# Kernel tuning notes

Measured on AMD Instinct MI355X. Metric: run time of the kernel, lower is better.

Reference implementation:

```python
import jax, jax.numpy as jnp
import numpy as np

N_SRC, N_TGT, K, L, C_OUT = 16384, 16384, 16, 128, 2
E = N_TGT * K
MIN_VAR = 1e-3   # adf.keep_variance_fn min variance (applied in Dropout)
DROP_P = 0.2
INV_SQRT2 = np.float32(1.0 / np.sqrt(2.0))
INV_SQRT2PI = np.float32(1.0 / np.sqrt(2.0 * np.pi))


def setup_inputs() -> dict:
    key = jax.random.key(0)
    ks = jax.random.split(key, 12)
    pos_source = jax.random.uniform(ks[0], (N_SRC, 3), jnp.float32)
    pos_target = jax.random.uniform(ks[1], (N_TGT, 3), jnp.float32)
    latents = jax.random.normal(ks[2], (N_SRC, L), jnp.float32)
    var = jax.random.uniform(ks[3], (N_SRC, L), jnp.float32)
    # KNN-style edge list: each target has K source neighbors
    row = jnp.repeat(jnp.arange(N_TGT, dtype=jnp.int32), K)          # [E] target idx
    col = jax.random.randint(ks[4], (E,), 0, N_SRC, jnp.int32)       # [E] source idx
    occupancies = jax.random.randint(ks[5], (N_TGT,), 0, 2, jnp.int32)
    # fixed inverted-dropout mask (deterministic stand-in for adf.Dropout training mask)
    drop_mask = (jax.random.uniform(ks[6], (E, L)) >= DROP_P).astype(jnp.float32) / (1.0 - DROP_P)
    def init_w(k, sh):
        return jax.random.normal(k, sh, jnp.float32) * np.float32(1.0 / np.sqrt(sh[-1]))
    W_in = init_w(ks[7], (L, L + 3)); b_in = jnp.zeros((L,), jnp.float32)
    W1 = init_w(ks[8], (L, L)); b1 = jnp.zeros((L,), jnp.float32)
    W2 = init_w(ks[9], (L, L)); b2 = jnp.zeros((L,), jnp.float32)
    W_out = init_w(ks[10], (C_OUT, L)); b_out = jnp.zeros((C_OUT,), jnp.float32)
    return dict(pos_source=pos_source, pos_target=pos_target, latents=latents, var=var,
                drop_mask=drop_mask, W_in=W_in, b_in=b_in, W1=W1, b1=b1, W2=W2, b2=b2,
                W_out=W_out, b_out=b_out, row=row, col=col, occupancies=occupancies)


def _adf_linear(m, v, W, b):
    # ADF Linear: mean -> affine; variance -> through squared weights, no bias
    return m @ W.T + b, v @ (W * W).T


def _adf_relu(m, v):
    # ADF ReLU moment matching (Gast & Roth); clamp var for sqrt stability
    v = jnp.maximum(v, 1e-6)
    std = jnp.sqrt(v)
    r = m / std
    cdf = 0.5 * (1.0 + jax.lax.erf(r * INV_SQRT2))
    pdf = jnp.exp(-0.5 * r * r) * INV_SQRT2PI
    m_out = m * cdf + std * pdf
    v_out = (m * m + v) * cdf + m * std * pdf - m_out * m_out
    return m_out, v_out


def reference(pos_source, pos_target, latents, var, drop_mask, W_in, b_in, W1, b1, W2, b2, W_out, b_out, row, col, occupancies):
    pos_rel = pos_target[row] - pos_source[col]                    # [E,3]
    m = jnp.concatenate([latents[col], pos_rel], axis=1)           # [E,L+3]
    v = jnp.concatenate([var[col], pos_rel], axis=1)               # [E,L+3] (faithful: pos_rel reused as 'variance')
    m, v = _adf_linear(m, v, W_in, b_in)
    for W, b in ((W1, b1), (W2, b2)):
        m, v = _adf_relu(m, v)
        m, v = _adf_linear(m, v, W, b)
    # ADF dropout with keep_variance_fn
    m = m * drop_mask
    v = v * drop_mask * drop_mask + MIN_VAR
    m, v = _adf_linear(m, v, W_out, b_out)                         # [E,2]
    preds = m[:, 0]
    aleatoric = jnp.abs(v[:, 0]).mean()
    occ_gt = occupancies[row].astype(jnp.float32)
    # stable binary_cross_entropy_with_logits, mean reduction
    recons_loss = jnp.mean(jnp.maximum(preds, 0.0) - preds * occ_gt + jnp.log1p(jnp.exp(-jnp.abs(preds))))
    return preds, aleatoric, recons_loss, occ_gt
```

## Files before the change

kernel.cpp:

```cpp
#include <hip/hip_runtime.h>
#include <math.h>

#define E_TOT 262144
#define N_SRC 16384
#define LDIM  128
#define MIN_VARF 0.001f
#define INV_SQRT2PIF 0.3989422804014327f
#define EPB   128
#define NBLK  (E_TOT / EPB)

typedef _Float16 half8  __attribute__((ext_vector_type(8)));
typedef __fp16   fp16x2 __attribute__((ext_vector_type(2)));
typedef float    f32x4  __attribute__((ext_vector_type(4)));
typedef float    f32x2  __attribute__((ext_vector_type(2)));
typedef unsigned int uint2v __attribute__((ext_vector_type(2)));

#define BIAS_OFF  256
#define WOUT_OFF  1792
#define BOUT_OFF  2816
#define PART_OFF  4096
#define PK_L0     36864
#define PK_L1     77824
#define PK_L2     110592
#define LAT16_OFF 143360
#define VAR16_OFF 4337664
#define WS_NEED   8531968

__device__ __forceinline__ unsigned int pkrtz(float a, float b) {
    union { fp16x2 h; unsigned int u; } z;
    z.h = __builtin_amdgcn_cvt_pkrtz(a, b);
    return z.u;
}
__device__ __forceinline__ half8 to_h8(f32x4 a, f32x4 b) {
    union { half8 h; unsigned int u[4]; } z;
    z.u[0] = pkrtz(a[0], a[1]); z.u[1] = pkrtz(a[2], a[3]);
    z.u[2] = pkrtz(b[0], b[1]); z.u[3] = pkrtz(b[2], b[3]);
    return z.h;
}
__device__ __forceinline__ half8 ch_to_h8(uint2v lo, uint2v hi) {
    union { half8 h; unsigned int u[4]; } z;
    z.u[0] = lo[0]; z.u[1] = lo[1]; z.u[2] = hi[0]; z.u[3] = hi[1];
    return z.h;
}

__device__ __forceinline__ void adf_relu(float& m, float& v) {
    float vv = fmaxf(v, 1e-6f);
    float is = __builtin_amdgcn_rsqf(vv);
    float sd = vv * is;
    float r  = m * is;
    float qq = 0.5f * r * r;
    float e  = __expf(-qq);
    float sp = sd * e * INV_SQRT2PIF;
    const float P = 0.23165247f;
    float t  = __builtin_amdgcn_rcpf(fmaf(fabsf(r), P, 1.0f));
    float poly = t * fmaf(t, fmaf(t, fmaf(t, fmaf(t, 1.061405429f, -1.453152027f),
                                          1.421413741f), -0.284496736f), 0.254829592f);
    float erfa = fmaf(-poly, e, 1.0f);
    float cdf  = fmaf(copysignf(0.5f, r), erfa, 0.5f);
    float mo = fmaf(m, cdf, sp);
    float vo = fmaf(fmaf(m, m, vv), cdf, fmaf(m, sp, -mo * mo));
    m = mo; v = vo;
}

__global__ void prep_pack(const float* __restrict__ latents, const float* __restrict__ varr,
                          char* __restrict__ ws)
{
    int idx = blockIdx.x * 256 + threadIdx.x;
    const int half = idx >> 18;
    const int j    = idx & 262143;
    const float* src = (half ? varr : latents) + (long)j * 8;
    char* dst = ws + (half ? VAR16_OFF : LAT16_OFF) + (long)j * 16;
    f32x4 a = *(const f32x4*)(src);
    f32x4 b = *(const f32x4*)(src + 4);
    half8 hv;
#pragma unroll
    for (int k = 0; k < 4; ++k) { hv[k] = (_Float16)a[k]; hv[k + 4] = (_Float16)b[k]; }
    *(half8*)dst = hv;
}

__global__ void prep(const float* __restrict__ W_in, const float* __restrict__ b_in,
                     const float* __restrict__ W1,   const float* __restrict__ b1,
                     const float* __restrict__ W2,   const float* __restrict__ b2,
                     const float* __restrict__ W_out,const float* __restrict__ b_out,
                     char* __restrict__ ws)
{
    int idx = blockIdx.x * 256 + threadIdx.x;
    if (idx < 6656) {
        const float* W; long dstoff; int entry; bool lin;
        if (idx < 2560)      { entry = idx;        W = W_in; dstoff = PK_L0; lin = true;  }
        else if (idx < 4608) { entry = idx - 2560; W = W1;   dstoff = PK_L1; lin = false; }
        else                 { entry = idx - 4608; W = W2;   dstoff = PK_L2; lin = false; }
        int ks   = entry >> 9;
        int rest = entry & 511;
        int t    = rest >> 6;
        int lane = rest & 63;
        int rowi = t * 16 + (lane & 15);
        int gp   = lane >> 4;
        half8 hv;
        if (lin) {
            int k0 = ks * 32 + gp * 8;
#pragma unroll
            for (int j = 0; j < 8; ++j) {
                int k = k0 + j;
                hv[j] = (_Float16)((k < 131) ? W[rowi * 131 + k] : 0.0f);
            }
        } else {
#pragma unroll
            for (int j = 0; j < 8; ++j) {
                int k = (2 * ks + (j >= 4 ? 1 : 0)) * 16 + 4 * gp + (j & 3);
                hv[j] = (_Float16)W[rowi * 128 + k];
            }
        }
        *(half8*)(ws + dstoff + (long)entry * 16) = hv;
    } else if (idx < 6656 + 384) {
        int j = idx - 6656; int layer = j >> 7; int pidx = j & 127;
        int gg = pidx >> 5, t = (pidx >> 2) & 7, r = pidx & 3;
        int n = t * 16 + gg * 4 + r;
        const float* b = layer == 0 ? b_in : (layer == 1 ? b1 : b2);
        ((float*)(ws + BIAS_OFF))[layer * 128 + pidx] = b[n];
    } else if (idx < 6656 + 384 + 256) {
        int j = idx - 6656 - 384; int path = j >> 7; int pidx = j & 127;
        int gg = pidx >> 5, t = (pidx >> 2) & 7, r = pidx & 3;
        int n = t * 16 + gg * 4 + r;
        float v = W_out[n];
        if (path) v = v * v;
        ((float*)(ws + WOUT_OFF))[path * 128 + pidx] = v;
    } else if (idx == 6656 + 384 + 256) {
        ((float*)(ws + BOUT_OFF))[0] = b_out[0];
    }
}

__device__ __forceinline__ void epi_reg(const f32x4* am, const f32x4* av, const f32x4* bp,
                                        uint2v* chm, uint2v* chv)
{
#pragma unroll
    for (int t = 0; t < 8; ++t) {
        f32x4 b4 = bp[t];
        float m0 = am[t][0] + b4[0], m1 = am[t][1] + b4[1];
        float m2 = am[t][2] + b4[2], m3 = am[t][3] + b4[3];
        float v0 = av[t][0], v1 = av[t][1], v2 = av[t][2], v3 = av[t][3];
        adf_relu(m0, v0); adf_relu(m1, v1); adf_relu(m2, v2); adf_relu(m3, v3);
        uint2v sm = {pkrtz(m0, m1), pkrtz(m2, m3)};
        uint2v sv = {pkrtz(v0, v1), pkrtz(v2, v3)};
        chm[t] = sm; chv[t] = sv;
    }
}

template <bool PACKED>
__global__ void __launch_bounds__(256, 2)
interp_main(const float* __restrict__ pos_source, const float* __restrict__ pos_target,
            const float* __restrict__ latents,    const float* __restrict__ varr,
            const float* __restrict__ drop_mask,
            const int* __restrict__ row, const int* __restrict__ col, const int* __restrict__ occ,
            float* __restrict__ out, char* __restrict__ ws)
{
    __shared__ float wred[4][2];

    const int tid  = threadIdx.x;
    const int lane = tid & 63;
    const int w    = tid >> 6;
    const int q    = lane & 15;
    const int g    = lane >> 4;
    const int g8   = g * 8;
    const int er0  = w * 32 + q;
    const int er1  = er0 + 16;
    const int ge0  = blockIdx.x * EPB + er0;
    const int ge1  = ge0 + 16;

    const int c0 = col[ge0], c1 = col[ge1];
    const int r0 = row[ge0], r1 = row[ge1];
    const float occf0 = (float)occ[r0];
    const float occf1 = (float)occ[r1];
    const float px0 = pos_target[r0 * 3 + 0] - pos_source[c0 * 3 + 0];
    const float py0 = pos_target[r0 * 3 + 1] - pos_source[c0 * 3 + 1];
    const float pz0 = pos_target[r0 * 3 + 2] - pos_source[c0 * 3 + 2];
    const float px1 = pos_target[r1 * 3 + 0] - pos_source[c1 * 3 + 0];
    const float py1 = pos_target[r1 * 3 + 1] - pos_source[c1 * 3 + 1];
    const float pz1 = pos_target[r1 * 3 + 2] - pos_source[c1 * 3 + 2];

    f32x4 acm0[8], acv0[8], acm1[8], acv1[8];
    const f32x4 zz = {0.0f, 0.0f, 0.0f, 0.0f};
#pragma unroll
    for (int t = 0; t < 8; ++t) { acm0[t] = zz; acv0[t] = zz; acm1[t] = zz; acv1[t] = zz; }

    uint2v chm0[8], chv0[8], chm1[8], chv1[8];

    {
        const char* pk = ws + PK_L0 + lane * 16;
#pragma unroll
        for (int ks = 0; ks < 4; ++ks) {
            half8 bm0, bv0, bm1, bv1;
            if (PACKED) {
                const long o0 = (long)c0 * 256 + ks * 64 + g8 * 2;
                const long o1 = (long)c1 * 256 + ks * 64 + g8 * 2;
                bm0 = *(const half8*)(ws + LAT16_OFF + o0);
                bv0 = *(const half8*)(ws + VAR16_OFF + o0);
                bm1 = *(const half8*)(ws + LAT16_OFF + o1);
                bv1 = *(const half8*)(ws + VAR16_OFF + o1);
            } else {
                const f32x4* a0 = (const f32x4*)(latents + (long)c0 * LDIM + ks * 32 + g8);
                const f32x4* s0 = (const f32x4*)(varr    + (long)c0 * LDIM + ks * 32 + g8);
                const f32x4* a1 = (const f32x4*)(latents + (long)c1 * LDIM + ks * 32 + g8);
                const f32x4* s1 = (const f32x4*)(varr    + (long)c1 * LDIM + ks * 32 + g8);
                bm0 = to_h8(a0[0], a0[1]); bv0 = to_h8(s0[0], s0[1]);
                bm1 = to_h8(a1[0], a1[1]); bv1 = to_h8(s1[0], s1[1]);
            }
            const char* pmk = pk + ks * 8192;
            __builtin_amdgcn_s_setprio(1);
#pragma unroll
            for (int t = 0; t < 8; ++t) {
                half8 am = *(const half8*)(pmk + t * 1024);
                half8 av = am * am;
                acm0[t] = __builtin_amdgcn_mfma_f32_16x16x32_f16(am, bm0, acm0[t], 0, 0, 0);
                acm1[t] = __builtin_amdgcn_mfma_f32_16x16x32_f16(am, bm1, acm1[t], 0, 0, 0);
                acv0[t] = __builtin_amdgcn_mfma_f32_16x16x32_f16(av, bv0, acv0[t], 0, 0, 0);
                acv1[t] = __builtin_amdgcn_mfma_f32_16x16x32_f16(av, bv1, acv1[t], 0, 0, 0);
            }
            __builtin_amdgcn_s_setprio(0);
        }
        half8 bp0 = {(_Float16)0.f, (_Float16)0.f, (_Float16)0.f, (_Float16)0.f,
                     (_Float16)0.f, (_Float16)0.f, (_Float16)0.f, (_Float16)0.f};
        half8 bp1 = bp0;
        if (g == 0) {
            bp0[0] = (_Float16)px0; bp0[1] = (_Float16)py0; bp0[2] = (_Float16)pz0;
            bp1[0] = (_Float16)px1; bp1[1] = (_Float16)py1; bp1[2] = (_Float16)pz1;
        }
        const char* pmk = pk + 4 * 8192;
        __builtin_amdgcn_s_setprio(1);
#pragma unroll
        for (int t = 0; t < 8; ++t) {
            half8 am = *(const half8*)(pmk + t * 1024);
            half8 av = am * am;
            acm0[t] = __builtin_amdgcn_mfma_f32_16x16x32_f16(am, bp0, acm0[t], 0, 0, 0);
            acm1[t] = __builtin_amdgcn_mfma_f32_16x16x32_f16(am, bp1, acm1[t], 0, 0, 0);
            acv0[t] = __builtin_amdgcn_mfma_f32_16x16x32_f16(av, bp0, acv0[t], 0, 0, 0);
            acv1[t] = __builtin_amdgcn_mfma_f32_16x16x32_f16(av, bp1, acv1[t], 0, 0, 0);
        }
        __builtin_amdgcn_s_setprio(0);
        const f32x4* bp = (const f32x4*)(ws + BIAS_OFF) + g8;
        epi_reg(acm0, acv0, bp, chm0, chv0);
        epi_reg(acm1, acv1, bp, chm1, chv1);
    }

#pragma unroll
    for (int layer = 1; layer < 3; ++layer) {
        const char* pk = ws + (layer == 1 ? PK_L1 : PK_L2) + lane * 16;
#pragma unroll
        for (int t = 0; t < 8; ++t) { acm0[t] = zz; acv0[t] = zz; acm1[t] = zz; acv1[t] = zz; }
#pragma unroll
        for (int ks = 0; ks < 4; ++ks) {
            half8 bm0 = ch_to_h8(chm0[2 * ks], chm0[2 * ks + 1]);
            half8 bv0 = ch_to_h8(chv0[2 * ks], chv0[2 * ks + 1]);
            half8 bm1 = ch_to_h8(chm1[2 * ks], chm1[2 * ks + 1]);
            half8 bv1 = ch_to_h8(chv1[2 * ks], chv1[2 * ks + 1]);
            const char* pmk = pk + ks * 8192;
            __builtin_amdgcn_s_setprio(1);
#pragma unroll
            for (int t = 0; t < 8; ++t) {
                half8 am = *(const half8*)(pmk + t * 1024);
                half8 av = am * am;
                acm0[t] = __builtin_amdgcn_mfma_f32_16x16x32_f16(am, bm0, acm0[t], 0, 0, 0);
                acm1[t] = __builtin_amdgcn_mfma_f32_16x16x32_f16(am, bm1, acm1[t], 0, 0, 0);
                acv0[t] = __builtin_amdgcn_mfma_f32_16x16x32_f16(av, bv0, acv0[t], 0, 0, 0);
                acv1[t] = __builtin_amdgcn_mfma_f32_16x16x32_f16(av, bv1, acv1[t], 0, 0, 0);
            }
            __builtin_amdgcn_s_setprio(0);
        }
        if (layer == 1) {
            const f32x4* bp = (const f32x4*)(ws + BIAS_OFF) + 32 + g8;
            epi_reg(acm0, acv0, bp, chm0, chv0);
            epi_reg(acm1, acv1, bp, chm1, chv1);
        }
    }

    {
        const f32x4* wmp = (const f32x4*)(ws + WOUT_OFF);
        const f32x4* bp  = (const f32x4*)(ws + BIAS_OFF) + 64 + g8;
        const f32x4* dm0 = (const f32x4*)(drop_mask + (size_t)ge0 * LDIM) + g;
        const f32x4* dm1 = (const f32x4*)(drop_mask + (size_t)ge1 * LDIM) + g;
        float pm0 = 0.f, pv0 = 0.f, pm1 = 0.f, pv1 = 0.f;
#pragma unroll
        for (int t = 0; t < 8; ++t) {
            f32x4 b4 = bp[t];
            f32x4 w4 = wmp[g8 + t];
            f32x4 s4 = wmp[32 + g8 + t];
            f32x4 d0 = __builtin_nontemporal_load(dm0 + t * 4);
            f32x4 d1 = __builtin_nontemporal_load(dm1 + t * 4);
#pragma unroll
            for (int j = 0; j < 4; ++j) {
                float m0 = (acm0[t][j] + b4[j]) * d0[j];
                float v0 = acv0[t][j] * d0[j] * d0[j] + MIN_VARF;
                float m1 = (acm1[t][j] + b4[j]) * d1[j];
                float v1 = acv1[t][j] * d1[j] * d1[j] + MIN_VARF;
                pm0 = fmaf(w4[j], m0, pm0); pv0 = fmaf(s4[j], v0, pv0);
                pm1 = fmaf(w4[j], m1, pm1); pv1 = fmaf(s4[j], v1, pv1);
            }
        }
        pm0 += __shfl_xor(pm0, 16, 64); pm0 += __shfl_xor(pm0, 32, 64);
        pv0 += __shfl_xor(pv0, 16, 64); pv0 += __shfl_xor(pv0, 32, 64);
        pm1 += __shfl_xor(pm1, 16, 64); pm1 += __shfl_xor(pm1, 32, 64);
        pv1 += __shfl_xor(pv1, 16, 64); pv1 += __shfl_xor(pv1, 32, 64);
        float bout = *(const float*)(ws + BOUT_OFF);
        float p0 = pm0 + bout;
        float p1 = pm1 + bout;
        if (lane < 16) {
            out[ge0] = p0;            out[ge1] = p1;
            out[E_TOT + 2 + ge0] = occf0;
            out[E_TOT + 2 + ge1] = occf1;
        }
        float a0 = fabsf(p0), a1 = fabsf(p1);
        float loss = fmaxf(p0, 0.f) - p0 * occf0 + __logf(1.0f + __expf(-a0))
                   + fmaxf(p1, 0.f) - p1 * occf1 + __logf(1.0f + __expf(-a1));
        float al = fabsf(pv0) + fabsf(pv1);
#pragma unroll
        for (int off = 1; off < 16; off <<= 1) {
            al   += __shfl_xor(al, off, 64);
            loss += __shfl_xor(loss, off, 64);
        }
        if (lane == 0) { wred[w][0] = al; wred[w][1] = loss; }
    }
    __syncthreads();
    if (tid == 0) {
        f32x2 s;
        s[0] = wred[0][0] + wred[1][0] + wred[2][0] + wred[3][0];
        s[1] = wred[0][1] + wred[1][1] + wred[2][1] + wred[3][1];
        *((f32x2*)(ws + PART_OFF) + blockIdx.x) = s;
    }
}

__global__ void __launch_bounds__(256)
interp_finalize(const char* __restrict__ ws, float* __restrict__ out)
{
    __shared__ float sal[4], sls[4];
    const int tid  = threadIdx.x;
    const int lane = tid & 63;
    const int w    = tid >> 6;
    float al = 0.0f, ls = 0.0f;
    const f32x2* part = (const f32x2*)(ws + PART_OFF);
    for (int i = tid; i < NBLK; i += 256) {
        f32x2 p = part[i];
        al += p[0]; ls += p[1];
    }
#pragma unroll
    for (int off = 1; off < 64; off <<= 1) {
        al += __shfl_xor(al, off, 64);
        ls += __shfl_xor(ls, off, 64);
    }
    if (lane == 0) { sal[w] = al; sls[w] = ls; }
    __syncthreads();
    if (tid == 0) {
        const float inv = 1.0f / (float)E_TOT;
        out[E_TOT]     = (sal[0] + sal[1] + sal[2] + sal[3]) * inv;
        out[E_TOT + 1] = (sls[0] + sls[1] + sls[2] + sls[3]) * inv;
    }
}

extern "C" void kernel_launch(void* const* d_in, const int* in_sizes, int n_in,
                              void* d_out, int out_size, void* d_ws, size_t ws_size,
                              hipStream_t stream) {
    (void)in_sizes; (void)n_in; (void)out_size;
    const float* pos_source = (const float*)d_in[0];
    const float* pos_target = (const float*)d_in[1];
    const float* latents    = (const float*)d_in[2];
    const float* varr       = (const float*)d_in[3];
    const float* drop_mask  = (const float*)d_in[4];
    const float* W_in       = (const float*)d_in[5];
    const float* b_in       = (const float*)d_in[6];
    const float* W1         = (const float*)d_in[7];
    const float* b1         = (const float*)d_in[8];
    const float* W2         = (const float*)d_in[9];
    const float* b2         = (const float*)d_in[10];
    const float* W_out      = (const float*)d_in[11];
    const float* b_out      = (const float*)d_in[12];
    const int*   row        = (const int*)d_in[13];
    const int*   col        = (const int*)d_in[14];
    const int*   occ        = (const int*)d_in[15];
    float* out = (float*)d_out;
    char*  ws  = (char*)d_ws;

    const bool packed = (ws_size >= (size_t)WS_NEED);
    prep<<<29, 256, 0, stream>>>(W_in, b_in, W1, b1, W2, b2, W_out, b_out, ws);
    if (packed) {
        prep_pack<<<2048, 256, 0, stream>>>(latents, varr, ws);
        interp_main<true><<<NBLK, 256, 0, stream>>>(
            pos_source, pos_target, latents, varr, drop_mask,
            row, col, occ, out, ws);
    } else {
        interp_main<false><<<NBLK, 256, 0, stream>>>(
            pos_source, pos_target, latents, varr, drop_mask,
            row, col, occ, out, ws);
    }
    interp_finalize<<<1, 256, 0, stream>>>(ws, out);
}
```

Before: 143.0 us.

## Interleave per-tile MFMA accumulation with ADF epilogue in hidden layers

Layers 1 and 2 now loop over output tiles on the outside and the K dimension on the inside. Each 16-wide output tile is accumulated fully and its ReLU/dropout epilogue runs right away, instead of all 32 accumulators being built before any epilogue starts. This shrinks the live accumulator set and lets VALU epilogue work overlap with MFMA work from the next tile. The drop_mask loads are hoisted ahead of the last layer's matmul to hide their latency. In exchange it needs separate next-layer register buffers (nm/nv), and it reloads weights in a different order, which may change register pressure and the instruction schedule.

```diff
diff --git a/kernel.cpp b/kernel.cpp
--- a/kernel.cpp
+++ b/kernel.cpp
@@ -60,6 +60,17 @@
     float mo = fmaf(m, cdf, sp);
     float vo = fmaf(fmaf(m, m, vv), cdf, fmaf(m, sp, -mo * mo));
     m = mo; v = vo;
+}
+
+__device__ __forceinline__ uint2v epi_t(f32x4 am, f32x4 av, f32x4 b4, uint2v* svo) {
+    float m0 = am[0] + b4[0], m1 = am[1] + b4[1];
+    float m2 = am[2] + b4[2], m3 = am[3] + b4[3];
+    float v0 = av[0], v1 = av[1], v2 = av[2], v3 = av[3];
+    adf_relu(m0, v0); adf_relu(m1, v1); adf_relu(m2, v2); adf_relu(m3, v3);
+    uint2v sm = {pkrtz(m0, m1), pkrtz(m2, m3)};
+    uint2v sv = {pkrtz(v0, v1), pkrtz(v2, v3)};
+    *svo = sv;
+    return sm;
 }
 
 __global__ void prep_pack(const float* __restrict__ latents, const float* __restrict__ varr,
@@ -130,22 +141,6 @@
     }
 }
 
-__device__ __forceinline__ void epi_reg(const f32x4* am, const f32x4* av, const f32x4* bp,
-                                        uint2v* chm, uint2v* chv)
-{
-#pragma unroll
-    for (int t = 0; t < 8; ++t) {
-        f32x4 b4 = bp[t];
-        float m0 = am[t][0] + b4[0], m1 = am[t][1] + b4[1];
-        float m2 = am[t][2] + b4[2], m3 = am[t][3] + b4[3];
-        float v0 = av[t][0], v1 = av[t][1], v2 = av[t][2], v3 = av[t][3];
-        adf_relu(m0, v0); adf_relu(m1, v1); adf_relu(m2, v2); adf_relu(m3, v3);
-        uint2v sm = {pkrtz(m0, m1), pkrtz(m2, m3)};
-        uint2v sv = {pkrtz(v0, v1), pkrtz(v2, v3)};
-        chm[t] = sm; chv[t] = sv;
-    }
-}
-
 template <bool PACKED>
 __global__ void __launch_bounds__(256, 2)
 interp_main(const float* __restrict__ pos_source, const float* __restrict__ pos_target,
@@ -178,14 +173,13 @@
     const float py1 = pos_target[r1 * 3 + 1] - pos_source[c1 * 3 + 1];
     const float pz1 = pos_target[r1 * 3 + 2] - pos_source[c1 * 3 + 2];
 
-    f32x4 acm0[8], acv0[8], acm1[8], acv1[8];
     const f32x4 zz = {0.0f, 0.0f, 0.0f, 0.0f};
-#pragma unroll
-    for (int t = 0; t < 8; ++t) { acm0[t] = zz; acv0[t] = zz; acm1[t] = zz; acv1[t] = zz; }
-
     uint2v chm0[8], chv0[8], chm1[8], chv1[8];
 
     {
+        f32x4 acm0[8], acv0[8], acm1[8], acv1[8];
+#pragma unroll
+        for (int t = 0; t < 8; ++t) { acm0[t] = zz; acv0[t] = zz; acm1[t] = zz; acv1[t] = zz; }
         const char* pk = ws + PK_L0 + lane * 16;
 #pragma unroll
         for (int ks = 0; ks < 4; ++ks) {
@@ -238,60 +232,83 @@
         }
         __builtin_amdgcn_s_setprio(0);
         const f32x4* bp = (const f32x4*)(ws + BIAS_OFF) + g8;
-        epi_reg(acm0, acv0, bp, chm0, chv0);
-        epi_reg(acm1, acv1, bp, chm1, chv1);
-    }
-
-#pragma unroll
-    for (int layer = 1; layer < 3; ++layer) {
-        const char* pk = ws + (layer == 1 ? PK_L1 : PK_L2) + lane * 16;
-#pragma unroll
-        for (int t = 0; t < 8; ++t) { acm0[t] = zz; acv0[t] = zz; acm1[t] = zz; acv1[t] = zz; }
-#pragma unroll
-        for (int ks = 0; ks < 4; ++ks) {
-            half8 bm0 = ch_to_h8(chm0[2 * ks], chm0[2 * ks + 1]);
-            half8 bv0 = ch_to_h8(chv0[2 * ks], chv0[2 * ks + 1]);
-            half8 bm1 = ch_to_h8(chm1[2 * ks], chm1[2 * ks + 1]);
-            half8 bv1 = ch_to_h8(chv1[2 * ks], chv1[2 * ks + 1]);
-            const char* pmk = pk + ks * 8192;
+#pragma unroll
+        for (int t = 0; t < 8; ++t) {
+            chm0[t] = epi_t(acm0[t], acv0[t], bp[t], &chv0[t]);
+            chm1[t] = epi_t(acm1[t], acv1[t], bp[t], &chv1[t]);
+        }
+    }
+
+    uint2v nm0[8], nv0[8], nm1[8], nv1[8];
+    {
+        const char* pk = ws + PK_L1 + lane * 16;
+        const f32x4* bp = (const f32x4*)(ws + BIAS_OFF) + 32 + g8;
+#pragma unroll
+        for (int t = 0; t < 8; ++t) {
+            f32x4 am0 = zz, av0 = zz, am1 = zz, av1 = zz;
             __builtin_amdgcn_s_setprio(1);
 #pragma unroll
-            for (int t = 0; t < 8; ++t) {
-                half8 am = *(const half8*)(pmk + t * 1024);
-                half8 av = am * am;
-                acm0[t] = __builtin_amdgcn_mfma_f32_16x16x32_f16(am, bm0, acm0[t], 0, 0, 0);
-                acm1[t] = __builtin_amdgcn_mfma_f32_16x16x32_f16(am, bm1, acm1[t], 0, 0, 0);
-                acv0[t] = __builtin_amdgcn_mfma_f32_16x16x32_f16(av, bv0, acv0[t], 0, 0, 0);
-                acv1[t] = __builtin_amdgcn_mfma_f32_16x16x32_f16(av, bv1, acv1[t], 0, 0, 0);
+            for (int ks = 0; ks < 4; ++ks) {
+                half8 wA = *(const half8*)(pk + ks * 8192 + t * 1024);
+                half8 wV = wA * wA;
+                half8 bm0 = ch_to_h8(chm0[2 * ks], chm0[2 * ks + 1]);
+                half8 bv0 = ch_to_h8(chv0[2 * ks], chv0[2 * ks + 1]);
+                half8 bm1 = ch_to_h8(chm1[2 * ks], chm1[2 * ks + 1]);
+                half8 bv1 = ch_to_h8(chv1[2 * ks], chv1[2 * ks + 1]);
+                am0 = __builtin_amdgcn_mfma_f32_16x16x32_f16(wA, bm0, am0, 0, 0, 0);
+                am1 = __builtin_amdgcn_mfma_f32_16x16x32_f16(wA, bm1, am1, 0, 0, 0);
+                av0 = __builtin_amdgcn_mfma_f32_16x16x32_f16(wV, bv0, av0, 0, 0, 0);
+                av1 = __builtin_amdgcn_mfma_f32_16x16x32_f16(wV, bv1, av1, 0, 0, 0);
             }
             __builtin_amdgcn_s_setprio(0);
-        }
-        if (layer == 1) {
-            const f32x4* bp = (const f32x4*)(ws + BIAS_OFF) + 32 + g8;
-            epi_reg(acm0, acv0, bp, chm0, chv0);
-            epi_reg(acm1, acv1, bp, chm1, chv1);
+            f32x4 b4 = bp[t];
+            nm0[t] = epi_t(am0, av0, b4, &nv0[t]);
+            nm1[t] = epi_t(am1, av1, b4, &nv1[t]);
         }
     }
 
     {
+        const f32x4* dm0 = (const f32x4*)(drop_mask + (size_t)ge0 * LDIM) + g;
+        const f32x4* dm1 = (const f32x4*)(drop_mask + (size_t)ge1 * LDIM) + g;
+        f32x4 md0[8], md1[8];
+#pragma unroll
+        for (int t = 0; t < 8; ++t) {
+            md0[t] = __builtin_nontemporal_load(dm0 + t * 4);
+            md1[t] = __builtin_nontemporal_load(dm1 + t * 4);
+        }
+        const char* pk = ws + PK_L2 + lane * 16;
         const f32x4* wmp = (const f32x4*)(ws + WOUT_OFF);
         const f32x4* bp  = (const f32x4*)(ws + BIAS_OFF) + 64 + g8;
-        const f32x4* dm0 = (const f32x4*)(drop_mask + (size_t)ge0 * LDIM) + g;
-        const f32x4* dm1 = (const f32x4*)(drop_mask + (size_t)ge1 * LDIM) + g;
         float pm0 = 0.f, pv0 = 0.f, pm1 = 0.f, pv1 = 0.f;
 #pragma unroll
         for (int t = 0; t < 8; ++t) {
+            f32x4 am0 = zz, av0 = zz, am1 = zz, av1 = zz;
+            __builtin_amdgcn_s_setprio(1);
+#pragma unroll
+            for (int ks = 0; ks < 4; ++ks) {
+                half8 wA = *(const half8*)(pk + ks * 8192 + t * 1024);
+                half8 wV = wA * wA;
+                half8 bm0 = ch_to_h8(nm0[2 * ks], nm0[2 * ks + 1]);
+                half8 bv0 = ch_to_h8(nv0[2 * ks], nv0[2 * ks + 1]);
+                half8 bm1 = ch_to_h8(nm1[2 * ks], nm1[2 * ks + 1]);
+                half8 bv1 = ch_to_h8(nv1[2 * ks], nv1[2 * ks + 1]);
+                am0 = __builtin_amdgcn_mfma_f32_16x16x32_f16(wA, bm0, am0, 0, 0, 0);
+                am1 = __builtin_amdgcn_mfma_f32_16x16x32_f16(wA, bm1, am1, 0, 0, 0);
+                av0 = __builtin_amdgcn_mfma_f32_16x16x32_f16(wV, bv0, av0, 0, 0, 0);
+                av1 = __builtin_amdgcn_mfma_f32_16x16x32_f16(wV, bv1, av1, 0, 0, 0);
+            }
+            __builtin_amdgcn_s_setprio(0);
             f32x4 b4 = bp[t];
             f32x4 w4 = wmp[g8 + t];
             f32x4 s4 = wmp[32 + g8 + t];
-            f32x4 d0 = __builtin_nontemporal_load(dm0 + t * 4);
-            f32x4 d1 = __builtin_nontemporal_load(dm1 + t * 4);
+            f32x4 d0 = md0[t];
+            f32x4 d1 = md1[t];
 #pragma unroll
             for (int j = 0; j < 4; ++j) {
-                float m0 = (acm0[t][j] + b4[j]) * d0[j];
-                float v0 = acv0[t][j] * d0[j] * d0[j] + MIN_VARF;
-                float m1 = (acm1[t][j] + b4[j]) * d1[j];
-                float v1 = acv1[t][j] * d1[j] * d1[j] + MIN_VARF;
+                float m0 = (am0[j] + b4[j]) * d0[j];
+                float v0 = av0[j] * d0[j] * d0[j] + MIN_VARF;
+                float m1 = (am1[j] + b4[j]) * d1[j];
+                float v1 = av1[j] * d1[j] * d1[j] + MIN_VARF;
                 pm0 = fmaf(w4[j], m0, pm0); pv0 = fmaf(s4[j], v0, pv0);
                 pm1 = fmaf(w4[j], m1, pm1); pv1 = fmaf(s4[j], v1, pv1);
             }
```

New measurement: 149.0 us. 4.2% more time.
